# Kernel tuning notes

Measured on AMD Instinct MI355X. Metric: run time of the kernel, lower is better.

Reference implementation:

```python
import jax, jax.numpy as jnp
import numpy as np

B, S, H = 32, 2048, 512

def setup_inputs() -> dict:
    key = jax.random.key(0)
    k1, k2, k3, k4 = jax.random.split(key, 4)
    Y = jax.random.normal(k1, (B, S, H), dtype=jnp.float32)
    mask_Y = jnp.ones((B, S), dtype=jnp.float32)
    W = jax.random.normal(k2, (H, H), dtype=jnp.float32)
    b = jax.random.normal(k3, (H,), dtype=jnp.float32)
    w = jax.random.normal(k4, (H,), dtype=jnp.float32)
    return {"Y": Y, "mask_Y": mask_Y, "W": W, "b": b, "w": w}

def reference(Y, mask_Y, W, b, w):
    # u: [B,S,H] = tanh(Y @ W + b)
    u = jnp.tanh(jnp.einsum('bsh,hd->bsd', Y, W) + b)
    # scores: [B,S] = u . w, masked with large negative additive bias
    scores = jnp.einsum('bsh,h->bs', u, w) - 1000.0 * (1.0 - mask_Y)
    alpha = jax.nn.softmax(scores, axis=1)  # [B,S]
    # c_star: [B,H] = attention-weighted sum of Y
    c_star = jnp.einsum('bs,bsh->bh', alpha, Y)
    return c_star
```

## Files before the change

kernel.cpp:

```cpp
#include <hip/hip_runtime.h>
#include <hip/hip_bf16.h>


#define Bsz 32
#define Ssz 2048
#define Hsz 512
#define Msz (Bsz * Ssz)

using half8   = __attribute__((ext_vector_type(8))) _Float16;
using floatx4 = __attribute__((ext_vector_type(4))) float;

__device__ __forceinline__ void llds16(void* l, const void* g) {
  __builtin_amdgcn_global_load_lds((const __attribute__((address_space(1))) void*)g,
                                   (__attribute__((address_space(3))) void*)l, 16, 0, 0);
}

__device__ __forceinline__ float fast_tanh(float x) {
  const float e = __expf(2.f * x);
  return 1.f - 2.f / (e + 1.f);
}

__global__ __launch_bounds__(256) void wsplit_k(const float* __restrict__ W,
                                                _Float16* __restrict__ Wt) {
  __shared__ float tile[32][33];
  const int bx = blockIdx.x & 15, by = blockIdx.x >> 4;
  const int tx = threadIdx.x & 31, ty = threadIdx.x >> 5;
#pragma unroll
  for (int i = 0; i < 4; ++i)
    tile[ty + 8 * i][tx] = W[(size_t)(by * 32 + ty + 8 * i) * Hsz + bx * 32 + tx];
  __syncthreads();
#pragma unroll
  for (int i = 0; i < 4; ++i) {
    const int n = bx * 32 + ty + 8 * i;
    const int k = by * 32 + tx;
    Wt[(size_t)n * Hsz + k] = (_Float16)tile[tx][ty + 8 * i];
  }
}

__global__ __launch_bounds__(256, 3) void gemm_score_k(const float* __restrict__ Y,
                                                       const _Float16* __restrict__ Wt,
                                                       const float* __restrict__ bvec,
                                                       const float* __restrict__ wvec,
                                                       float* __restrict__ scores4) {
  __shared__ __align__(16) _Float16 Bs[2][128 * 32];
  const int tid = threadIdx.x;
  const int lane = tid & 63, wv = tid >> 6;
  const int lr = lane & 15, lq = lane >> 4;
  const int g = blockIdx.x;
  const int x = g & 7, q = g >> 3;
  const int nblk = q & 3;
  const int mblk = (q >> 2) * 8 + x;

  const _Float16* bW = Wt + (size_t)nblk * 128 * Hsz;

  int bL[2]; const _Float16* bG[2];
#pragma unroll
  for (int i = 0; i < 2; ++i) {
    const int cb = i * 256 + wv * 64;
    const int p = cb + lane;
    const int row = p >> 2;
    const int gc = (p & 3) ^ ((row >> 1) & 3);
    bL[i] = cb * 8;
    bG[i] = bW + (size_t)row * Hsz + gc * 8;
  }

  const float* aR0 = Y + (size_t)(mblk * 128 + wv * 32 + lr) * Hsz + lq * 8;
  const float* aR1 = aR0 + (size_t)16 * Hsz;

  floatx4 acc[2][8];
#pragma unroll
  for (int rf = 0; rf < 2; ++rf)
#pragma unroll
    for (int cf = 0; cf < 8; ++cf)
      acc[rf][cf] = (floatx4){0.f, 0.f, 0.f, 0.f};

#pragma unroll
  for (int i = 0; i < 2; ++i) { llds16(&Bs[0][bL[i]], bG[i]); bG[i] += 32; }
  __builtin_amdgcn_sched_barrier(0);
  float4 f00 = *(const float4*)(aR0);
  float4 f01 = *(const float4*)(aR0 + 4);
  float4 f10 = *(const float4*)(aR1);
  float4 f11 = *(const float4*)(aR1 + 4);
  __builtin_amdgcn_sched_barrier(0);
#pragma unroll
  for (int i = 0; i < 2; ++i) { llds16(&Bs[1][bL[i]], bG[i]); bG[i] += 32; }

  for (int it = 0; it < 16; ++it) {
    if (it < 15) asm volatile("s_waitcnt vmcnt(6)" ::: "memory");
    else         asm volatile("s_waitcnt vmcnt(4)" ::: "memory");
    __builtin_amdgcn_s_barrier();

    half8 a0, a1;
    a0[0] = (_Float16)f00.x; a0[1] = (_Float16)f00.y;
    a0[2] = (_Float16)f00.z; a0[3] = (_Float16)f00.w;
    a0[4] = (_Float16)f01.x; a0[5] = (_Float16)f01.y;
    a0[6] = (_Float16)f01.z; a0[7] = (_Float16)f01.w;
    a1[0] = (_Float16)f10.x; a1[1] = (_Float16)f10.y;
    a1[2] = (_Float16)f10.z; a1[3] = (_Float16)f10.w;
    a1[4] = (_Float16)f11.x; a1[5] = (_Float16)f11.y;
    a1[6] = (_Float16)f11.z; a1[7] = (_Float16)f11.w;

    if (it < 15) {
      const int k1 = (it + 1) * 32;
      f00 = *(const float4*)(aR0 + k1);
      f01 = *(const float4*)(aR0 + k1 + 4);
      f10 = *(const float4*)(aR1 + k1);
      f11 = *(const float4*)(aR1 + k1 + 4);
    }

    const _Float16* Bsb = Bs[it & 1];
#pragma unroll
    for (int cf = 0; cf < 8; ++cf) {
      const int nr = cf * 16 + lr;
      const half8 bf = *(const half8*)&Bsb[nr * 32 + (lq ^ ((nr >> 1) & 3)) * 8];
      acc[0][cf] = __builtin_amdgcn_mfma_f32_16x16x32_f16(a0, bf, acc[0][cf], 0, 0, 0);
      acc[1][cf] = __builtin_amdgcn_mfma_f32_16x16x32_f16(a1, bf, acc[1][cf], 0, 0, 0);
    }

    asm volatile("s_waitcnt lgkmcnt(0)" ::: "memory");
    __builtin_amdgcn_s_barrier();
    if (it < 14) {
#pragma unroll
      for (int i = 0; i < 2; ++i) { llds16(&Bs[it & 1][bL[i]], bG[i]); bG[i] += 32; }
    }
  }

  float bb[8], ww[8];
#pragma unroll
  for (int cf = 0; cf < 8; ++cf) {
    const int col = nblk * 128 + cf * 16 + lr;
    bb[cf] = bvec[col];
    ww[cf] = wvec[col];
  }
#pragma unroll
  for (int rf = 0; rf < 2; ++rf) {
#pragma unroll
    for (int r = 0; r < 4; ++r) {
      float v = 0.f;
#pragma unroll
      for (int cf = 0; cf < 8; ++cf)
        v += fast_tanh(acc[rf][cf][r] + bb[cf]) * ww[cf];
      v += __shfl_xor(v, 1, 16);
      v += __shfl_xor(v, 2, 16);
      v += __shfl_xor(v, 4, 16);
      v += __shfl_xor(v, 8, 16);
      if (lr == 0)
        scores4[(size_t)nblk * Msz + mblk * 128 + wv * 32 + rf * 16 + lq * 4 + r] = v;
    }
  }
}

__global__ __launch_bounds__(1024) void red_k(const float* __restrict__ scores4,
                                              const float* __restrict__ mask,
                                              float* __restrict__ ssum,
                                              float* __restrict__ minv) {
  const int b = blockIdx.x, t = threadIdx.x;
  const int lane = t & 63, w = t >> 6;
  __shared__ float rm[16], rs[16];
  float v[2];
  float mx = -3.4e38f;
#pragma unroll
  for (int i = 0; i < 2; ++i) {
    const int idx = b * Ssz + i * 1024 + t;
    float s = scores4[idx] + scores4[Msz + idx] + scores4[2 * Msz + idx] + scores4[3 * Msz + idx];
    s -= 1000.f * (1.f - mask[idx]);
    ssum[idx] = s;
    v[i] = s;
    mx = fmaxf(mx, s);
  }
  for (int off = 32; off > 0; off >>= 1) mx = fmaxf(mx, __shfl_xor(mx, off, 64));
  if (lane == 0) rm[w] = mx;
  __syncthreads();
  mx = rm[0];
#pragma unroll
  for (int i = 1; i < 16; ++i) mx = fmaxf(mx, rm[i]);
  float sum = __expf(v[0] - mx) + __expf(v[1] - mx);
  for (int off = 32; off > 0; off >>= 1) sum += __shfl_xor(sum, off, 64);
  if (lane == 0) rs[w] = sum;
  __syncthreads();
  if (t == 0) {
    float tot = rs[0];
#pragma unroll
    for (int i = 1; i < 16; ++i) tot += rs[i];
    minv[b * 2]     = mx;
    minv[b * 2 + 1] = 1.f / tot;
  }
}

__global__ __launch_bounds__(256) void wsum_k(const float* __restrict__ ssum,
                                              const float* __restrict__ minv,
                                              const float* __restrict__ Y,
                                              float* __restrict__ out) {
  const int b = blockIdx.x >> 5, sc = blockIdx.x & 31;
  const int t = threadIdx.x, lane = t & 63, wv = t >> 6;
  __shared__ float part[4 * 512];
  const int s0 = sc * 64 + wv * 16;
  const float mx  = minv[b * 2];
  const float inv = minv[b * 2 + 1];
  const float* sl = ssum + b * Ssz + s0;
  const float4* Yb = (const float4*)(Y + ((size_t)b * Ssz + s0) * Hsz);
  float a0 = 0.f, a1 = 0.f, a2 = 0.f, a3 = 0.f, a4 = 0.f, a5 = 0.f, a6 = 0.f, a7 = 0.f;
#pragma unroll 4
  for (int r = 0; r < 16; ++r) {
    const float a = __expf(sl[r] - mx) * inv;
    const float4 y0 = Yb[r * 128 + lane * 2];
    const float4 y1 = Yb[r * 128 + lane * 2 + 1];
    a0 = fmaf(a, y0.x, a0); a1 = fmaf(a, y0.y, a1);
    a2 = fmaf(a, y0.z, a2); a3 = fmaf(a, y0.w, a3);
    a4 = fmaf(a, y1.x, a4); a5 = fmaf(a, y1.y, a5);
    a6 = fmaf(a, y1.z, a6); a7 = fmaf(a, y1.w, a7);
  }
  part[wv * 512 + 0 * 64 + lane] = a0;
  part[wv * 512 + 1 * 64 + lane] = a1;
  part[wv * 512 + 2 * 64 + lane] = a2;
  part[wv * 512 + 3 * 64 + lane] = a3;
  part[wv * 512 + 4 * 64 + lane] = a4;
  part[wv * 512 + 5 * 64 + lane] = a5;
  part[wv * 512 + 6 * 64 + lane] = a6;
  part[wv * 512 + 7 * 64 + lane] = a7;
  __syncthreads();
#pragma unroll
  for (int i = 0; i < 2; ++i) {
    const int h = i * 256 + t;
    const int idx = (h & 7) * 64 + (h >> 3);
    atomicAdd(&out[(size_t)b * Hsz + h],
              part[idx] + part[512 + idx] + part[1024 + idx] + part[1536 + idx]);
  }
}

extern "C" void kernel_launch(void* const* d_in, const int* in_sizes, int n_in,
                              void* d_out, int out_size, void* d_ws, size_t ws_size,
                              hipStream_t stream) {
  (void)in_sizes; (void)n_in; (void)out_size; (void)ws_size;
  const float* Y    = (const float*)d_in[0];
  const float* mask = (const float*)d_in[1];
  const float* W    = (const float*)d_in[2];
  const float* bvec = (const float*)d_in[3];
  const float* wvec = (const float*)d_in[4];
  float* out = (float*)d_out;

  char* ws = (char*)d_ws;
  _Float16* Wt   = (_Float16*)ws;
  float* scores4 = (float*)(ws + ((size_t)1 << 20));
  float* ssum    = (float*)(ws + ((size_t)2 << 20));
  float* minv    = (float*)(ws + ((size_t)2304 << 10));

  hipMemsetAsync(out, 0, (size_t)Bsz * Hsz * sizeof(float), stream);
  wsplit_k<<<256, 256, 0, stream>>>(W, Wt);
  gemm_score_k<<<(Msz / 128) * 4, 256, 0, stream>>>(Y, Wt, bvec, wvec, scores4);
  red_k<<<Bsz, 1024, 0, stream>>>(scores4, mask, ssum, minv);
  wsum_k<<<Bsz * 32, 256, 0, stream>>>(ssum, minv, Y, out);
}
```

Baseline: 273.7 us.

## Pre-convert Y to fp16 once, deepen A prefetch, replace atomics with two-pass reduction

Adds a pass that converts Y to fp16 in workspace, so the GEMM and the weighted-sum kernels read half the bytes and skip the per-tile conversion. The GEMM loop is unrolled by two with a two-stage register prefetch of A, and the launch-bounds occupancy hint is dropped. The atomic weighted sum is replaced by per-chunk partials plus a second reduction kernel, which removes the memset. The cost is an extra full read of Y in fp32 plus a 64 MiB fp16 write, the fp16 path only runs when the workspace is large enough, and the weighted sum now uses fp16-rounded Y, which adds error.

```diff
diff --git a/kernel.cpp b/kernel.cpp
--- a/kernel.cpp
+++ b/kernel.cpp
@@ -18,6 +18,24 @@
 __device__ __forceinline__ float fast_tanh(float x) {
   const float e = __expf(2.f * x);
   return 1.f - 2.f / (e + 1.f);
+}
+
+__global__ __launch_bounds__(256) void ysplit_k(const float* __restrict__ Y,
+                                                _Float16* __restrict__ Yh) {
+  const int t = blockIdx.x * 256 + threadIdx.x;
+  const float4* src = (const float4*)Y;
+#pragma unroll
+  for (int i = 0; i < 8; ++i) {
+    const size_t gidx = (size_t)i * 524288 + t;
+    const float4 lo = src[gidx * 2];
+    const float4 hi = src[gidx * 2 + 1];
+    half8 h;
+    h[0] = (_Float16)lo.x; h[1] = (_Float16)lo.y;
+    h[2] = (_Float16)lo.z; h[3] = (_Float16)lo.w;
+    h[4] = (_Float16)hi.x; h[5] = (_Float16)hi.y;
+    h[6] = (_Float16)hi.z; h[7] = (_Float16)hi.w;
+    *(half8*)&Yh[gidx * 8] = h;
+  }
 }
 
 __global__ __launch_bounds__(256) void wsplit_k(const float* __restrict__ W,
@@ -37,11 +55,12 @@
   }
 }
 
-__global__ __launch_bounds__(256, 3) void gemm_score_k(const float* __restrict__ Y,
-                                                       const _Float16* __restrict__ Wt,
-                                                       const float* __restrict__ bvec,
-                                                       const float* __restrict__ wvec,
-                                                       float* __restrict__ scores4) {
+template <bool FP16A>
+__global__ __launch_bounds__(256) void gemm_score_k(const void* __restrict__ Yv,
+                                                    const _Float16* __restrict__ Wt,
+                                                    const float* __restrict__ bvec,
+                                                    const float* __restrict__ wvec,
+                                                    float* __restrict__ scores4) {
   __shared__ __align__(16) _Float16 Bs[2][128 * 32];
   const int tid = threadIdx.x;
   const int lane = tid & 63, wv = tid >> 6;
@@ -64,8 +83,11 @@
     bG[i] = bW + (size_t)row * Hsz + gc * 8;
   }
 
-  const float* aR0 = Y + (size_t)(mblk * 128 + wv * 32 + lr) * Hsz + lq * 8;
-  const float* aR1 = aR0 + (size_t)16 * Hsz;
+  const int arow = mblk * 128 + wv * 32 + lr;
+  const _Float16* aH0 = (const _Float16*)Yv + (size_t)arow * Hsz + lq * 8;
+  const _Float16* aH1 = aH0 + (size_t)16 * Hsz;
+  const float*    aF0 = (const float*)Yv + (size_t)arow * Hsz + lq * 8;
+  const float*    aF1 = aF0 + (size_t)16 * Hsz;
 
   floatx4 acc[2][8];
 #pragma unroll
@@ -74,54 +96,119 @@
     for (int cf = 0; cf < 8; ++cf)
       acc[rf][cf] = (floatx4){0.f, 0.f, 0.f, 0.f};
 
+  half8  hA0, hA1, hB0, hB1;
+  float4 fA00, fA01, fA10, fA11;
+  float4 fB00, fB01, fB10, fB11;
+
 #pragma unroll
   for (int i = 0; i < 2; ++i) { llds16(&Bs[0][bL[i]], bG[i]); bG[i] += 32; }
-  __builtin_amdgcn_sched_barrier(0);
-  float4 f00 = *(const float4*)(aR0);
-  float4 f01 = *(const float4*)(aR0 + 4);
-  float4 f10 = *(const float4*)(aR1);
-  float4 f11 = *(const float4*)(aR1 + 4);
-  __builtin_amdgcn_sched_barrier(0);
+  if constexpr (FP16A) {
+    hA0 = *(const half8*)(aH0); hA1 = *(const half8*)(aH1);
+  } else {
+    fA00 = *(const float4*)(aF0);     fA01 = *(const float4*)(aF0 + 4);
+    fA10 = *(const float4*)(aF1);     fA11 = *(const float4*)(aF1 + 4);
+  }
 #pragma unroll
   for (int i = 0; i < 2; ++i) { llds16(&Bs[1][bL[i]], bG[i]); bG[i] += 32; }
-
-  for (int it = 0; it < 16; ++it) {
-    if (it < 15) asm volatile("s_waitcnt vmcnt(6)" ::: "memory");
-    else         asm volatile("s_waitcnt vmcnt(4)" ::: "memory");
-    __builtin_amdgcn_s_barrier();
-
-    half8 a0, a1;
-    a0[0] = (_Float16)f00.x; a0[1] = (_Float16)f00.y;
-    a0[2] = (_Float16)f00.z; a0[3] = (_Float16)f00.w;
-    a0[4] = (_Float16)f01.x; a0[5] = (_Float16)f01.y;
-    a0[6] = (_Float16)f01.z; a0[7] = (_Float16)f01.w;
-    a1[0] = (_Float16)f10.x; a1[1] = (_Float16)f10.y;
-    a1[2] = (_Float16)f10.z; a1[3] = (_Float16)f10.w;
-    a1[4] = (_Float16)f11.x; a1[5] = (_Float16)f11.y;
-    a1[6] = (_Float16)f11.z; a1[7] = (_Float16)f11.w;
-
-    if (it < 15) {
-      const int k1 = (it + 1) * 32;
-      f00 = *(const float4*)(aR0 + k1);
-      f01 = *(const float4*)(aR0 + k1 + 4);
-      f10 = *(const float4*)(aR1 + k1);
-      f11 = *(const float4*)(aR1 + k1 + 4);
-    }
-
-    const _Float16* Bsb = Bs[it & 1];
-#pragma unroll
-    for (int cf = 0; cf < 8; ++cf) {
-      const int nr = cf * 16 + lr;
-      const half8 bf = *(const half8*)&Bsb[nr * 32 + (lq ^ ((nr >> 1) & 3)) * 8];
-      acc[0][cf] = __builtin_amdgcn_mfma_f32_16x16x32_f16(a0, bf, acc[0][cf], 0, 0, 0);
-      acc[1][cf] = __builtin_amdgcn_mfma_f32_16x16x32_f16(a1, bf, acc[1][cf], 0, 0, 0);
-    }
-
-    asm volatile("s_waitcnt lgkmcnt(0)" ::: "memory");
-    __builtin_amdgcn_s_barrier();
-    if (it < 14) {
-#pragma unroll
-      for (int i = 0; i < 2; ++i) { llds16(&Bs[it & 1][bL[i]], bG[i]); bG[i] += 32; }
+  if constexpr (FP16A) {
+    hB0 = *(const half8*)(aH0 + 32); hB1 = *(const half8*)(aH1 + 32);
+  } else {
+    fB00 = *(const float4*)(aF0 + 32); fB01 = *(const float4*)(aF0 + 36);
+    fB10 = *(const float4*)(aF1 + 32); fB11 = *(const float4*)(aF1 + 36);
+  }
+
+#pragma unroll 1
+  for (int ii = 0; ii < 8; ++ii) {
+    {
+      const int it = 2 * ii;
+      if constexpr (FP16A) { asm volatile("s_waitcnt vmcnt(6)" ::: "memory"); }
+      else                 { asm volatile("s_waitcnt vmcnt(10)" ::: "memory"); }
+      __builtin_amdgcn_s_barrier();
+
+      half8 a0, a1;
+      if constexpr (FP16A) {
+        a0 = hA0; a1 = hA1;
+      } else {
+        a0[0] = (_Float16)fA00.x; a0[1] = (_Float16)fA00.y;
+        a0[2] = (_Float16)fA00.z; a0[3] = (_Float16)fA00.w;
+        a0[4] = (_Float16)fA01.x; a0[5] = (_Float16)fA01.y;
+        a0[6] = (_Float16)fA01.z; a0[7] = (_Float16)fA01.w;
+        a1[0] = (_Float16)fA10.x; a1[1] = (_Float16)fA10.y;
+        a1[2] = (_Float16)fA10.z; a1[3] = (_Float16)fA10.w;
+        a1[4] = (_Float16)fA11.x; a1[5] = (_Float16)fA11.y;
+        a1[6] = (_Float16)fA11.z; a1[7] = (_Float16)fA11.w;
+      }
+      if (it < 14) {
+        const int k2 = (it + 2) * 32;
+        if constexpr (FP16A) {
+          hA0 = *(const half8*)(aH0 + k2); hA1 = *(const half8*)(aH1 + k2);
+        } else {
+          fA00 = *(const float4*)(aF0 + k2);     fA01 = *(const float4*)(aF0 + k2 + 4);
+          fA10 = *(const float4*)(aF1 + k2);     fA11 = *(const float4*)(aF1 + k2 + 4);
+        }
+      }
+      const _Float16* Bsb = Bs[0];
+#pragma unroll
+      for (int cf = 0; cf < 8; ++cf) {
+        const int nr = cf * 16 + lr;
+        const half8 bf = *(const half8*)&Bsb[nr * 32 + (lq ^ ((nr >> 1) & 3)) * 8];
+        acc[0][cf] = __builtin_amdgcn_mfma_f32_16x16x32_f16(a0, bf, acc[0][cf], 0, 0, 0);
+        acc[1][cf] = __builtin_amdgcn_mfma_f32_16x16x32_f16(a1, bf, acc[1][cf], 0, 0, 0);
+      }
+      asm volatile("s_waitcnt lgkmcnt(0)" ::: "memory");
+      __builtin_amdgcn_s_barrier();
+      if (it < 14) {
+#pragma unroll
+        for (int i = 0; i < 2; ++i) { llds16(&Bs[0][bL[i]], bG[i]); bG[i] += 32; }
+      }
+    }
+    {
+      const int it = 2 * ii + 1;
+      if (it < 15) {
+        if constexpr (FP16A) { asm volatile("s_waitcnt vmcnt(6)" ::: "memory"); }
+        else                 { asm volatile("s_waitcnt vmcnt(10)" ::: "memory"); }
+      } else {
+        if constexpr (FP16A) { asm volatile("s_waitcnt vmcnt(2)" ::: "memory"); }
+        else                 { asm volatile("s_waitcnt vmcnt(4)" ::: "memory"); }
+      }
+      __builtin_amdgcn_s_barrier();
+
+      half8 a0, a1;
+      if constexpr (FP16A) {
+        a0 = hB0; a1 = hB1;
+      } else {
+        a0[0] = (_Float16)fB00.x; a0[1] = (_Float16)fB00.y;
+        a0[2] = (_Float16)fB00.z; a0[3] = (_Float16)fB00.w;
+        a0[4] = (_Float16)fB01.x; a0[5] = (_Float16)fB01.y;
+        a0[6] = (_Float16)fB01.z; a0[7] = (_Float16)fB01.w;
+        a1[0] = (_Float16)fB10.x; a1[1] = (_Float16)fB10.y;
+        a1[2] = (_Float16)fB10.z; a1[3] = (_Float16)fB10.w;
+        a1[4] = (_Float16)fB11.x; a1[5] = (_Float16)fB11.y;
+        a1[6] = (_Float16)fB11.z; a1[7] = (_Float16)fB11.w;
+      }
+      if (it < 14) {
+        const int k2 = (it + 2) * 32;
+        if constexpr (FP16A) {
+          hB0 = *(const half8*)(aH0 + k2); hB1 = *(const half8*)(aH1 + k2);
+        } else {
+          fB00 = *(const float4*)(aF0 + k2);     fB01 = *(const float4*)(aF0 + k2 + 4);
+          fB10 = *(const float4*)(aF1 + k2);     fB11 = *(const float4*)(aF1 + k2 + 4);
+        }
+      }
+      const _Float16* Bsb = Bs[1];
+#pragma unroll
+      for (int cf = 0; cf < 8; ++cf) {
+        const int nr = cf * 16 + lr;
+        const half8 bf = *(const half8*)&Bsb[nr * 32 + (lq ^ ((nr >> 1) & 3)) * 8];
+        acc[0][cf] = __builtin_amdgcn_mfma_f32_16x16x32_f16(a0, bf, acc[0][cf], 0, 0, 0);
+        acc[1][cf] = __builtin_amdgcn_mfma_f32_16x16x32_f16(a1, bf, acc[1][cf], 0, 0, 0);
+      }
+      asm volatile("s_waitcnt lgkmcnt(0)" ::: "memory");
+      __builtin_amdgcn_s_barrier();
+      if (it < 14) {
+#pragma unroll
+        for (int i = 0; i < 2; ++i) { llds16(&Bs[1][bL[i]], bG[i]); bG[i] += 32; }
+      }
     }
   }
 
@@ -187,51 +274,71 @@
   }
 }
 
-__global__ __launch_bounds__(256) void wsum_k(const float* __restrict__ ssum,
-                                              const float* __restrict__ minv,
-                                              const float* __restrict__ Y,
-                                              float* __restrict__ out) {
-  const int b = blockIdx.x >> 5, sc = blockIdx.x & 31;
+template <bool FP16Y>
+__global__ __launch_bounds__(256) void wsum1_k(const float* __restrict__ ssum,
+                                               const float* __restrict__ minv,
+                                               const void* __restrict__ Yv,
+                                               float* __restrict__ partial) {
+  const int b = blockIdx.x >> 6, g = blockIdx.x & 63;
   const int t = threadIdx.x, lane = t & 63, wv = t >> 6;
-  __shared__ float part[4 * 512];
-  const int s0 = sc * 64 + wv * 16;
+  __shared__ float part[4][512];
+  const int s0 = g * 32 + wv * 8;
   const float mx  = minv[b * 2];
   const float inv = minv[b * 2 + 1];
   const float* sl = ssum + b * Ssz + s0;
-  const float4* Yb = (const float4*)(Y + ((size_t)b * Ssz + s0) * Hsz);
-  float a0 = 0.f, a1 = 0.f, a2 = 0.f, a3 = 0.f, a4 = 0.f, a5 = 0.f, a6 = 0.f, a7 = 0.f;
-#pragma unroll 4
-  for (int r = 0; r < 16; ++r) {
-    const float a = __expf(sl[r] - mx) * inv;
-    const float4 y0 = Yb[r * 128 + lane * 2];
-    const float4 y1 = Yb[r * 128 + lane * 2 + 1];
-    a0 = fmaf(a, y0.x, a0); a1 = fmaf(a, y0.y, a1);
-    a2 = fmaf(a, y0.z, a2); a3 = fmaf(a, y0.w, a3);
-    a4 = fmaf(a, y1.x, a4); a5 = fmaf(a, y1.y, a5);
-    a6 = fmaf(a, y1.z, a6); a7 = fmaf(a, y1.w, a7);
-  }
-  part[wv * 512 + 0 * 64 + lane] = a0;
-  part[wv * 512 + 1 * 64 + lane] = a1;
-  part[wv * 512 + 2 * 64 + lane] = a2;
-  part[wv * 512 + 3 * 64 + lane] = a3;
-  part[wv * 512 + 4 * 64 + lane] = a4;
-  part[wv * 512 + 5 * 64 + lane] = a5;
-  part[wv * 512 + 6 * 64 + lane] = a6;
-  part[wv * 512 + 7 * 64 + lane] = a7;
+
+  float acc[8];
+#pragma unroll
+  for (int i = 0; i < 8; ++i) acc[i] = 0.f;
+
+  if constexpr (FP16Y) {
+    const _Float16* Yb = (const _Float16*)Yv + ((size_t)b * Ssz + s0) * Hsz + lane * 8;
+#pragma unroll
+    for (int j = 0; j < 8; ++j) {
+      const float a = __expf(sl[j] - mx) * inv;
+      const half8 y = *(const half8*)(Yb + (size_t)j * Hsz);
+#pragma unroll
+      for (int i = 0; i < 8; ++i) acc[i] = fmaf(a, (float)y[i], acc[i]);
+    }
+  } else {
+    const float* Yb = (const float*)Yv + ((size_t)b * Ssz + s0) * Hsz + lane * 8;
+#pragma unroll
+    for (int j = 0; j < 8; ++j) {
+      const float a = __expf(sl[j] - mx) * inv;
+      const float4 y0 = *(const float4*)(Yb + (size_t)j * Hsz);
+      const float4 y1 = *(const float4*)(Yb + (size_t)j * Hsz + 4);
+      acc[0] = fmaf(a, y0.x, acc[0]); acc[1] = fmaf(a, y0.y, acc[1]);
+      acc[2] = fmaf(a, y0.z, acc[2]); acc[3] = fmaf(a, y0.w, acc[3]);
+      acc[4] = fmaf(a, y1.x, acc[4]); acc[5] = fmaf(a, y1.y, acc[5]);
+      acc[6] = fmaf(a, y1.z, acc[6]); acc[7] = fmaf(a, y1.w, acc[7]);
+    }
+  }
+  *(float4*)&part[wv][lane * 8]     = (float4){acc[0], acc[1], acc[2], acc[3]};
+  *(float4*)&part[wv][lane * 8 + 4] = (float4){acc[4], acc[5], acc[6], acc[7]};
   __syncthreads();
 #pragma unroll
   for (int i = 0; i < 2; ++i) {
     const int h = i * 256 + t;
-    const int idx = (h & 7) * 64 + (h >> 3);
-    atomicAdd(&out[(size_t)b * Hsz + h],
-              part[idx] + part[512 + idx] + part[1024 + idx] + part[1536 + idx]);
-  }
+    partial[((size_t)(b * 64 + g)) * Hsz + h] =
+        part[0][h] + part[1][h] + part[2][h] + part[3][h];
+  }
+}
+
+__global__ __launch_bounds__(256) void wsum2_k(const float* __restrict__ partial,
+                                               float* __restrict__ out) {
+  const int b = blockIdx.x >> 1;
+  const int h = (blockIdx.x & 1) * 256 + threadIdx.x;
+  float s = 0.f;
+#pragma unroll 8
+  for (int g = 0; g < 64; ++g)
+    s += partial[((size_t)(b * 64 + g)) * Hsz + h];
+  out[b * Hsz + h] = s;
 }
 
 extern "C" void kernel_launch(void* const* d_in, const int* in_sizes, int n_in,
                               void* d_out, int out_size, void* d_ws, size_t ws_size,
                               hipStream_t stream) {
-  (void)in_sizes; (void)n_in; (void)out_size; (void)ws_size;
+  (void)in_sizes; (void)n_in; (void)out_size;
   const float* Y    = (const float*)d_in[0];
   const float* mask = (const float*)d_in[1];
   const float* W    = (const float*)d_in[2];
@@ -244,10 +351,20 @@
   float* scores4 = (float*)(ws + ((size_t)1 << 20));
   float* ssum    = (float*)(ws + ((size_t)2 << 20));
   float* minv    = (float*)(ws + ((size_t)2304 << 10));
-
-  hipMemsetAsync(out, 0, (size_t)Bsz * Hsz * sizeof(float), stream);
+  float* partial = (float*)(ws + ((size_t)3 << 20));
+  _Float16* Yh   = (_Float16*)(ws + ((size_t)8 << 20));
+
+  const bool useH = ws_size >= ((size_t)72 << 20);
+
   wsplit_k<<<256, 256, 0, stream>>>(W, Wt);
-  gemm_score_k<<<(Msz / 128) * 4, 256, 0, stream>>>(Y, Wt, bvec, wvec, scores4);
+  if (useH) {
+    ysplit_k<<<2048, 256, 0, stream>>>(Y, Yh);
+    gemm_score_k<true><<<(Msz / 128) * 4, 256, 0, stream>>>(Yh, Wt, bvec, wvec, scores4);
+  } else {
+    gemm_score_k<false><<<(Msz / 128) * 4, 256, 0, stream>>>(Y, Wt, bvec, wvec, scores4);
+  }
   red_k<<<Bsz, 1024, 0, stream>>>(scores4, mask, ssum, minv);
-  wsum_k<<<Bsz * 32, 256, 0, stream>>>(ssum, minv, Y, out);
-}
+  if (useH) wsum1_k<true><<<Bsz * 64, 256, 0, stream>>>(ssum, minv, Yh, partial);
+  else      wsum1_k<false><<<Bsz * 64, 256, 0, stream>>>(ssum, minv, Y, partial);
+  wsum2_k<<<Bsz * 2, 256, 0, stream>>>(partial, out);
+}
```

Result: slower. 289.2 us (+5.7%).
